# Kernel optimization log

Hardware: AMD Instinct MI355X
Metric: run time of the kernel (lower is better)

The kernel has to match this reference:

```python
import jax, jax.numpy as jnp
import numpy as np
from math import ceil

EPS = 1e-5
K_NN = 4
RATIO = 0.8


def _bn(x, g, b, rm, rv):
    # BatchNorm1d in inference mode with running stats
    return (x - rm) * (g / jnp.sqrt(rv + EPS)) + b


def _mlp1(x, W, bias, g, b, rm, rv):
    # S(Linear, ReLU, BN)
    return _bn(jax.nn.relu(x @ W + bias), g, b, rm, rv)


def _knn_edges(pos, B, n, k):
    p = pos.reshape(B, n, -1)
    d2 = jnp.sum((p[:, :, None, :] - p[:, None, :, :]) ** 2, axis=-1)  # [B,n,n]
    d2 = d2 + jnp.eye(n, dtype=d2.dtype) * 1e10  # loop=False
    _, nbr = jax.lax.top_k(-d2, k)  # [B,n,k] k nearest neighbors j of node i
    off = (jnp.arange(B, dtype=jnp.int32) * n)[:, None, None]
    src = (nbr.astype(jnp.int32) + off).reshape(-1)  # sources j (x_j)
    dst = (jnp.broadcast_to(jnp.arange(n, dtype=jnp.int32)[None, :, None], (B, n, k)) + off).reshape(-1)  # targets i (x_i)
    return src, dst


def _edge_conv(x, src, dst, emask, N, W, bias, g, b, rm, rv):
    xi = x[dst]
    xj = x[src]
    m = _mlp1(jnp.concatenate([xi, xj - xi], axis=1), W, bias, g, b, rm, rv)
    m = m * emask[:, None]
    s = jax.ops.segment_sum(m, dst, num_segments=N)
    cnt = jax.ops.segment_sum(emask, dst, num_segments=N)
    return s / jnp.maximum(cnt, 1.0)[:, None]  # aggr='mean' (0 for isolated nodes)


def _topk_pool(x, src, dst, emask, w, B, n, k_keep):
    score = (x @ w) / jnp.linalg.norm(w)  # [B*n]
    top_sc, perm = jax.lax.top_k(score.reshape(B, n), k_keep)  # [B,k_keep]
    off = (jnp.arange(B, dtype=jnp.int32) * n)[:, None]
    perm_flat = (perm.astype(jnp.int32) + off).reshape(-1)
    x_new = x[perm_flat] * jnp.tanh(top_sc).reshape(-1)[:, None]
    old2new = jnp.full((B * n,), -1, dtype=jnp.int32).at[perm_flat].set(
        jnp.arange(B * k_keep, dtype=jnp.int32))
    ns, nd = old2new[src], old2new[dst]
    new_mask = emask * (ns >= 0).astype(emask.dtype) * (nd >= 0).astype(emask.dtype)
    return x_new, jnp.maximum(ns, 0), jnp.maximum(nd, 0), new_mask


def _forward(x, pos, B, n,
             W1, b1, g1, be1, rm1, rv1, pw1,
             W2, b2, g2, be2, rm2, rv2, pw2,
             W3, b3, g3, be3, rm3, rv3,
             Wc1, bc1, gc1, bec1, rmc1, rvc1,
             Wc2, bc2, gc2, bec2, rmc2, rvc2):
    src, dst = _knn_edges(pos, B, n, K_NN)
    emask = jnp.ones(src.shape[0], dtype=x.dtype)
    h = _edge_conv(x, src, dst, emask, B * n, W1, b1, g1, be1, rm1, rv1)
    k1 = ceil(RATIO * n)
    h, src, dst, emask = _topk_pool(h, src, dst, emask, pw1, B, n, k1)
    h = _edge_conv(h, src, dst, emask, B * k1, W2, b2, g2, be2, rm2, rv2)
    k2 = ceil(RATIO * k1)
    h, src, dst, emask = _topk_pool(h, src, dst, emask, pw2, B, k1, k2)
    h = _edge_conv(h, src, dst, emask, B * k2, W3, b3, g3, be3, rm3, rv3)
    gmp = h.reshape(B, k2, -1).mean(axis=1)  # global_mean_pool
    z = _mlp1(gmp, Wc1, bc1, gc1, bec1, rmc1, rvc1)
    z = _mlp1(z, Wc2, bc2, gc2, bec2, rmc2, rvc2)
    return jax.nn.sigmoid(z)[:, 0]


def setup_inputs() -> dict:
    key = jax.random.key(0)
    B, n, C = 256, 128, 53
    keys = iter(jax.random.split(key, 64))

    def nrm(shape, s=1.0):
        return jax.random.normal(next(keys), shape, jnp.float32) * s

    def lin(i, o):
        return nrm((i, o), 1.0 / np.sqrt(i)), nrm((o,), 0.01)

    def bnp(c):
        return (1.0 + nrm((c,), 0.1), nrm((c,), 0.1), nrm((c,), 0.1),
                0.5 + jax.random.uniform(next(keys), (c,), jnp.float32))

    inp = {"x": nrm((B * n, C)), "pos": nrm((B * n, 3))}
    inp["W1"], inp["b1"] = lin(106, 128)
    inp["g1"], inp["be1"], inp["rm1"], inp["rv1"] = bnp(128)
    inp["pw1"] = nrm((128,))
    inp["W2"], inp["b2"] = lin(256, 256)
    inp["g2"], inp["be2"], inp["rm2"], inp["rv2"] = bnp(256)
    inp["pw2"] = nrm((256,))
    inp["W3"], inp["b3"] = lin(512, 512)
    inp["g3"], inp["be3"], inp["rm3"], inp["rv3"] = bnp(512)
    inp["Wc1"], inp["bc1"] = lin(512, 512)
    inp["gc1"], inp["bec1"], inp["rmc1"], inp["rvc1"] = bnp(512)
    inp["Wc2"], inp["bc2"] = lin(512, 1)
    inp["gc2"], inp["bec2"], inp["rmc2"], inp["rvc2"] = bnp(1)
    inp["n_graphs"] = B
    inp["nodes_per_graph"] = n
    return inp


def reference(x, pos,
              W1, b1, g1, be1, rm1, rv1, pw1,
              W2, b2, g2, be2, rm2, rv2, pw2,
              W3, b3, g3, be3, rm3, rv3,
              Wc1, bc1, gc1, bec1, rmc1, rvc1,
              Wc2, bc2, gc2, bec2, rmc2, rvc2,
              n_graphs, nodes_per_graph):
    return _forward(x, pos, n_graphs, nodes_per_graph,
                    W1, b1, g1, be1, rm1, rv1, pw1,
                    W2, b2, g2, be2, rm2, rv2, pw2,
                    W3, b3, g3, be3, rm3, rv3,
                    Wc1, bc1, gc1, bec1, rmc1, rvc1,
                    Wc2, bc2, gc2, bec2, rmc2, rvc2)
```

## Files before the change

### kernel.cpp

```cpp
#include <hip/hip_runtime.h>
#include <hip/hip_bf16.h>
#include <math.h>

#define B_G  256
#define NPG  128
#define KNN_ 4
#define CIN  53
#define N1   32768
#define KP1  103
#define N2   26368
#define KP2  83
#define N3   21248
#define O1   128
#define O2   256
#define O3   512
#define EPSB 1e-5f

typedef __attribute__((ext_vector_type(8))) short bf16x8;
typedef __attribute__((ext_vector_type(4))) float f32x4;

__device__ inline ushort f2bf(float f) {
    unsigned u = __builtin_bit_cast(unsigned, f);
    u += 0x7fff + ((u >> 16) & 1);
    return (ushort)(u >> 16);
}
__device__ inline float bf2f(ushort h) {
    unsigned u = ((unsigned)h) << 16;
    return __builtin_bit_cast(float, u);
}

__global__ void pack_w_k(const float* __restrict__ W, float* __restrict__ Wp,
                         int Kd, int O) {
    int i = blockIdx.x * blockDim.x + threadIdx.x;
    int tot = Kd * 2 * O;
    if (i >= tot) return;
    int k = i / (2 * O), c = i % (2 * O);
    Wp[i] = (c < O) ? W[k * O + c] : W[(Kd + k) * O + (c - O)];
}

__global__ void pack_w3t_k(const float* __restrict__ W3,
                           ushort* __restrict__ BhT, ushort* __restrict__ BlT) {
    int i = blockIdx.x * blockDim.x + threadIdx.x;
    if (i >= 1024 * 256) return;
    int n = i >> 8, k = i & 255;
    float w = (n < 512) ? W3[(size_t)k * 512 + n] : W3[(size_t)(256 + k) * 512 + (n - 512)];
    ushort h = f2bf(w);
    BhT[i] = h;
    BlT[i] = f2bf(w - bf2f(h));
}

__global__ void norm_w_k(const float* __restrict__ pw, float* __restrict__ pwn, int O) {
    __shared__ float red[256];
    float s = 0.f;
    for (int c = threadIdx.x; c < O; c += 256) s += pw[c] * pw[c];
    red[threadIdx.x] = s;
    __syncthreads();
    for (int st = 128; st > 0; st >>= 1) {
        if (threadIdx.x < st) red[threadIdx.x] += red[threadIdx.x + st];
        __syncthreads();
    }
    float inv = 1.0f / sqrtf(red[0]);
    for (int c = threadIdx.x; c < O; c += 256) pwn[c] = pw[c] * inv;
}

__global__ void knn_k(const float* __restrict__ pos, int* __restrict__ nbr) {
    int g = blockIdx.x;
    int i = threadIdx.x;
    __shared__ float px[NPG], py[NPG], pz[NPG];
    const float* p = pos + (size_t)g * NPG * 3;
    px[i] = p[i * 3 + 0]; py[i] = p[i * 3 + 1]; pz[i] = p[i * 3 + 2];
    __syncthreads();
    float b0 = 1e30f, b1 = 1e30f, b2 = 1e30f, b3 = 1e30f;
    int   i0 = 0, i1 = 0, i2 = 0, i3 = 0;
    float xi = px[i], yi = py[i], zi = pz[i];
    for (int j = 0; j < NPG; ++j) {
        float dx = xi - px[j], dy = yi - py[j], dz = zi - pz[j];
        float d2 = dx * dx + dy * dy + dz * dz;
        if (j != i && d2 < b3) {
            if (d2 < b0) {
                b3 = b2; i3 = i2; b2 = b1; i2 = i1; b1 = b0; i1 = i0; b0 = d2; i0 = j;
            } else if (d2 < b1) {
                b3 = b2; i3 = i2; b2 = b1; i2 = i1; b1 = d2; i1 = j;
            } else if (d2 < b2) {
                b3 = b2; i3 = i2; b2 = d2; i2 = j;
            } else {
                b3 = d2; i3 = j;
            }
        }
    }
    int base = (g * NPG + i) * KNN_;
    nbr[base + 0] = g * NPG + i0;
    nbr[base + 1] = g * NPG + i1;
    nbr[base + 2] = g * NPG + i2;
    nbr[base + 3] = g * NPG + i3;
}

template <int VEC>
__global__ __launch_bounds__(256) void gemm128_k(
        const float* __restrict__ A, const float* __restrict__ Bm,
        float* __restrict__ Cm, int M, int N, int Kd, int lda) {
    __shared__ float As[16][128];
    __shared__ float Bs[16][128];
    const int tid = threadIdx.x;
    const int row0 = blockIdx.y * 128, col0 = blockIdx.x * 128;
    const int tx = tid & 15;
    const int ty = (tid >> 4) & 15;
    const int s_arow = tid >> 1, s_ak = (tid & 1) * 8;
    const int s_bk = tid >> 4, s_bc = (tid & 15) * 8;
    float acc[8][8] = {};
    for (int k0 = 0; k0 < Kd; k0 += 16) {
        if (VEC) {
            const float4* ap = (const float4*)(A + (size_t)(row0 + s_arow) * lda + k0 + s_ak);
            float4 a0 = ap[0], a1 = ap[1];
            As[s_ak + 0][s_arow] = a0.x; As[s_ak + 1][s_arow] = a0.y;
            As[s_ak + 2][s_arow] = a0.z; As[s_ak + 3][s_arow] = a0.w;
            As[s_ak + 4][s_arow] = a1.x; As[s_ak + 5][s_arow] = a1.y;
            As[s_ak + 6][s_arow] = a1.z; As[s_ak + 7][s_arow] = a1.w;
            const float4* bp = (const float4*)(Bm + (size_t)(k0 + s_bk) * N + col0 + s_bc);
            float4 b0 = bp[0], b1 = bp[1];
            *(float4*)&Bs[s_bk][s_bc] = b0;
            *(float4*)&Bs[s_bk][s_bc + 4] = b1;
        } else {
            #pragma unroll
            for (int s = 0; s < 8; ++s) {
                int kk = s_ak + s;
                As[kk][s_arow] = (k0 + kk < Kd)
                    ? A[(size_t)(row0 + s_arow) * lda + k0 + kk] : 0.f;
            }
            #pragma unroll
            for (int s = 0; s < 8; ++s) {
                Bs[s_bk][s_bc + s] = (k0 + s_bk < Kd)
                    ? Bm[(size_t)(k0 + s_bk) * N + col0 + s_bc + s] : 0.f;
            }
        }
        __syncthreads();
        #pragma unroll
        for (int kk = 0; kk < 16; ++kk) {
            float a[8], b[8];
            *(float4*)&a[0] = *(const float4*)&As[kk][ty * 4];
            *(float4*)&a[4] = *(const float4*)&As[kk][64 + ty * 4];
            *(float4*)&b[0] = *(const float4*)&Bs[kk][tx * 4];
            *(float4*)&b[4] = *(const float4*)&Bs[kk][64 + tx * 4];
            #pragma unroll
            for (int i = 0; i < 8; ++i)
                #pragma unroll
                for (int j = 0; j < 8; ++j)
                    acc[i][j] += a[i] * b[j];
        }
        __syncthreads();
    }
    #pragma unroll
    for (int i = 0; i < 8; ++i) {
        int r = row0 + ((i < 4) ? (ty * 4 + i) : (64 + ty * 4 + (i - 4)));
        size_t base = (size_t)r * N + col0;
        *(float4*)&Cm[base + tx * 4]      = *(float4*)&acc[i][0];
        *(float4*)&Cm[base + 64 + tx * 4] = *(float4*)&acc[i][4];
    }
}

#define LDK 40
__global__ __launch_bounds__(256) void gemm3_mfma_k(
        const ushort* __restrict__ Ah, const ushort* __restrict__ Al,
        const ushort* __restrict__ BhT, const ushort* __restrict__ BlT,
        float* __restrict__ Cm) {
    __shared__ ushort sAh[128][LDK], sAl[128][LDK], sBh[128][LDK], sBl[128][LDK];
    const int tid = threadIdx.x;
    const int row0 = blockIdx.y * 128, col0 = blockIdx.x * 128;
    const int w = tid >> 6, lane = tid & 63;
    const int wr = (w >> 1) * 64, wc = (w & 1) * 64;
    const int fr = lane & 15, fk = (lane >> 4) * 8;
    const int s_r = tid >> 2, s_c = (tid & 3) * 8;
    f32x4 acc[4][4] = {};
    for (int k0 = 0; k0 < 256; k0 += 32) {
        {
            size_t ga0 = (size_t)(row0 + s_r) * 256 + k0 + s_c;
            size_t ga1 = (size_t)(row0 + 64 + s_r) * 256 + k0 + s_c;
            *(uint4*)&sAh[s_r][s_c]      = *(const uint4*)&Ah[ga0];
            *(uint4*)&sAh[64 + s_r][s_c] = *(const uint4*)&Ah[ga1];
            *(uint4*)&sAl[s_r][s_c]      = *(const uint4*)&Al[ga0];
            *(uint4*)&sAl[64 + s_r][s_c] = *(const uint4*)&Al[ga1];
            size_t gb0 = (size_t)(col0 + s_r) * 256 + k0 + s_c;
            size_t gb1 = (size_t)(col0 + 64 + s_r) * 256 + k0 + s_c;
            *(uint4*)&sBh[s_r][s_c]      = *(const uint4*)&BhT[gb0];
            *(uint4*)&sBh[64 + s_r][s_c] = *(const uint4*)&BhT[gb1];
            *(uint4*)&sBl[s_r][s_c]      = *(const uint4*)&BlT[gb0];
            *(uint4*)&sBl[64 + s_r][s_c] = *(const uint4*)&BlT[gb1];
        }
        __syncthreads();
        bf16x8 fa_h[4], fa_l[4], fb_h[4], fb_l[4];
        #pragma unroll
        for (int mi = 0; mi < 4; ++mi) {
            fa_h[mi] = *(const bf16x8*)&sAh[wr + mi * 16 + fr][fk];
            fa_l[mi] = *(const bf16x8*)&sAl[wr + mi * 16 + fr][fk];
        }
        #pragma unroll
        for (int ni = 0; ni < 4; ++ni) {
            fb_h[ni] = *(const bf16x8*)&sBh[wc + ni * 16 + fr][fk];
            fb_l[ni] = *(const bf16x8*)&sBl[wc + ni * 16 + fr][fk];
        }
        #pragma unroll
        for (int mi = 0; mi < 4; ++mi)
            #pragma unroll
            for (int ni = 0; ni < 4; ++ni) {
                acc[mi][ni] = __builtin_amdgcn_mfma_f32_16x16x32_bf16(
                    fa_h[mi], fb_h[ni], acc[mi][ni], 0, 0, 0);
                acc[mi][ni] = __builtin_amdgcn_mfma_f32_16x16x32_bf16(
                    fa_h[mi], fb_l[ni], acc[mi][ni], 0, 0, 0);
                acc[mi][ni] = __builtin_amdgcn_mfma_f32_16x16x32_bf16(
                    fa_l[mi], fb_h[ni], acc[mi][ni], 0, 0, 0);
            }
        __syncthreads();
    }
    const int crow = (lane >> 4) * 4, ccol = lane & 15;
    #pragma unroll
    for (int mi = 0; mi < 4; ++mi)
        #pragma unroll
        for (int ni = 0; ni < 4; ++ni) {
            size_t base = (size_t)(row0 + wr + mi * 16 + crow) * 1024
                          + col0 + wc + ni * 16 + ccol;
            #pragma unroll
            for (int r = 0; r < 4; ++r)
                Cm[base + (size_t)r * 1024] = acc[mi][ni][r];
        }
}

__global__ void conv_agg_k(const float* __restrict__ AC, const int* __restrict__ edges,
                           const float* __restrict__ bias, const float* __restrict__ g,
                           const float* __restrict__ be, const float* __restrict__ rm,
                           const float* __restrict__ rv, float* __restrict__ out, int O) {
    int node = blockIdx.x;
    int c = threadIdx.x;
    int e0 = node * KNN_;
    int j0 = edges[e0 + 0], j1 = edges[e0 + 1], j2 = edges[e0 + 2], j3 = edges[e0 + 3];
    size_t s2O = (size_t)2 * O;
    float Ai = AC[(size_t)node * s2O + c];
    float Ci = AC[(size_t)node * s2O + O + c];
    float base = Ai - Ci + bias[c];
    float acc = 0.f; int cnt = 0;
    if (j0 >= 0) { acc += fmaxf(base + AC[(size_t)j0 * s2O + O + c], 0.f); ++cnt; }
    if (j1 >= 0) { acc += fmaxf(base + AC[(size_t)j1 * s2O + O + c], 0.f); ++cnt; }
    if (j2 >= 0) { acc += fmaxf(base + AC[(size_t)j2 * s2O + O + c], 0.f); ++cnt; }
    if (j3 >= 0) { acc += fmaxf(base + AC[(size_t)j3 * s2O + O + c], 0.f); ++cnt; }
    float h;
    if (cnt > 0) {
        float m = acc / (float)cnt;
        float sc = g[c] / sqrtf(rv[c] + EPSB);
        h = (m - rm[c]) * sc + be[c];
    } else {
        h = 0.f;
    }
    out[(size_t)node * O + c] = h;
}

__global__ void score_k(const float* __restrict__ h, const float* __restrict__ pwn,
                        float* __restrict__ sc, int Nl, int O) {
    int wid = (blockIdx.x * blockDim.x + threadIdx.x) >> 6;
    int lane = threadIdx.x & 63;
    if (wid >= Nl) return;
    float s = 0.f;
    for (int c = lane; c < O; c += 64) s += h[(size_t)wid * O + c] * pwn[c];
    #pragma unroll
    for (int off = 32; off > 0; off >>= 1) s += __shfl_down(s, off);
    if (lane == 0) sc[wid] = s;
}

__global__ void topk_rank_k(const float* __restrict__ sc, int n_l, int k_keep,
                            float* __restrict__ gate, int* __restrict__ perm,
                            int* __restrict__ o2n) {
    int g = blockIdx.x;
    int t = threadIdx.x;
    __shared__ float s[NPG];
    if (t < n_l) s[t] = sc[(size_t)g * n_l + t];
    __syncthreads();
    if (t >= n_l) return;
    float v = s[t];
    int rank = 0;
    for (int j = 0; j < n_l; ++j) {
        float vj = s[j];
        rank += (vj > v || (vj == v && j < t)) ? 1 : 0;
    }
    int gi = g * n_l + t;
    if (rank < k_keep) {
        int d = g * k_keep + rank;
        perm[d] = gi;
        gate[d] = tanhf(v);
        o2n[gi] = d;
    } else {
        o2n[gi] = -1;
    }
}

__global__ void gather_k(const float* __restrict__ h, const int* __restrict__ perm,
                         const float* __restrict__ gate, float* __restrict__ xo,
                         int total, int oshift) {
    int i = blockIdx.x * blockDim.x + threadIdx.x;
    if (i >= total) return;
    int d = i >> oshift, c = i & ((1 << oshift) - 1);
    xo[i] = h[((size_t)perm[d] << oshift) + c] * gate[d];
}

__global__ void gather_bf_k(const float* __restrict__ h, const int* __restrict__ perm,
                            const float* __restrict__ gate,
                            ushort* __restrict__ Ah, ushort* __restrict__ Al, int total) {
    int i = blockIdx.x * blockDim.x + threadIdx.x;
    if (i >= total) return;
    int d = i >> 8, c = i & 255;
    float v = h[((size_t)perm[d] << 8) + c] * gate[d];
    ushort hh = f2bf(v);
    Ah[i] = hh;
    Al[i] = f2bf(v - bf2f(hh));
}

__global__ void build_e2_k(const int* __restrict__ nbr, const int* __restrict__ perm1,
                           const int* __restrict__ o2n1, int* __restrict__ e2, int total) {
    int i = blockIdx.x * blockDim.x + threadIdx.x;
    if (i >= total) return;
    int u = i >> 2, kk = i & 3;
    e2[i] = o2n1[nbr[perm1[u] * KNN_ + kk]];
}

__global__ void build_e3_k(const int* __restrict__ e2, const int* __restrict__ perm2,
                           const int* __restrict__ o2n2, int* __restrict__ e3, int total) {
    int i = blockIdx.x * blockDim.x + threadIdx.x;
    if (i >= total) return;
    int v = i >> 2, kk = i & 3;
    int s1 = e2[perm2[v] * KNN_ + kk];
    e3[i] = (s1 >= 0) ? o2n2[s1] : -1;
}

__global__ void gmp_k(const float* __restrict__ h3, float* __restrict__ gmp) {
    int g = blockIdx.x, c = threadIdx.x;
    float s = 0.f;
    for (int r = 0; r < KP2; ++r) s += h3[((size_t)(g * KP2 + r)) * O3 + c];
    gmp[(size_t)g * O3 + c] = s / (float)KP2;
}

__global__ void mlpc_k(const float* __restrict__ X, const float* __restrict__ W,
                       const float* __restrict__ bias, const float* __restrict__ g,
                       const float* __restrict__ be, const float* __restrict__ rm,
                       const float* __restrict__ rv, float* __restrict__ out) {
    int b = blockIdx.x, o = threadIdx.x;
    __shared__ float xr[512];
    xr[o] = X[(size_t)b * 512 + o];
    __syncthreads();
    float acc = bias[o];
    for (int k = 0; k < 512; ++k) acc += xr[k] * W[(size_t)k * 512 + o];
    acc = fmaxf(acc, 0.f);
    float s = g[o] / sqrtf(rv[o] + EPSB);
    out[(size_t)b * 512 + o] = (acc - rm[o]) * s + be[o];
}

__global__ void final_k(const float* __restrict__ z1, const float* __restrict__ Wc2,
                        const float* __restrict__ bc2, const float* __restrict__ gc2,
                        const float* __restrict__ bec2, const float* __restrict__ rmc2,
                        const float* __restrict__ rvc2, float* __restrict__ out) {
    int b = blockIdx.x * blockDim.x + threadIdx.x;
    if (b >= B_G) return;
    float acc = bc2[0];
    for (int k = 0; k < 512; ++k) acc += z1[(size_t)b * 512 + k] * Wc2[k];
    acc = fmaxf(acc, 0.f);
    float s = gc2[0] / sqrtf(rvc2[0] + EPSB);
    float z = (acc - rmc2[0]) * s + bec2[0];
    out[b] = 1.f / (1.f + expf(-z));
}

extern "C" void kernel_launch(void* const* d_in, const int* in_sizes, int n_in,
                              void* d_out, int out_size, void* d_ws, size_t ws_size,
                              hipStream_t stream) {
    const float* x    = (const float*)d_in[0];
    const float* pos  = (const float*)d_in[1];
    const float* W1   = (const float*)d_in[2];
    const float* b1   = (const float*)d_in[3];
    const float* g1   = (const float*)d_in[4];
    const float* be1  = (const float*)d_in[5];
    const float* rm1  = (const float*)d_in[6];
    const float* rv1  = (const float*)d_in[7];
    const float* pw1  = (const float*)d_in[8];
    const float* W2   = (const float*)d_in[9];
    const float* b2   = (const float*)d_in[10];
    const float* g2   = (const float*)d_in[11];
    const float* be2  = (const float*)d_in[12];
    const float* rm2  = (const float*)d_in[13];
    const float* rv2  = (const float*)d_in[14];
    const float* pw2  = (const float*)d_in[15];
    const float* W3   = (const float*)d_in[16];
    const float* b3   = (const float*)d_in[17];
    const float* g3   = (const float*)d_in[18];
    const float* be3  = (const float*)d_in[19];
    const float* rm3  = (const float*)d_in[20];
    const float* rv3  = (const float*)d_in[21];
    const float* Wc1  = (const float*)d_in[22];
    const float* bc1  = (const float*)d_in[23];
    const float* gc1  = (const float*)d_in[24];
    const float* bec1 = (const float*)d_in[25];
    const float* rmc1 = (const float*)d_in[26];
    const float* rvc1 = (const float*)d_in[27];
    const float* Wc2  = (const float*)d_in[28];
    const float* bc2  = (const float*)d_in[29];
    const float* gc2  = (const float*)d_in[30];
    const float* bec2 = (const float*)d_in[31];
    const float* rmc2 = (const float*)d_in[32];
    const float* rvc2 = (const float*)d_in[33];
    float* out = (float*)d_out;

    char* ws = (char*)d_ws;
    size_t off = 0;
    auto take = [&](size_t bytes) { size_t o = off; off = (off + bytes + 255) & ~(size_t)255; return o; };
    size_t o_nbr   = take((size_t)N1 * KNN_ * 4);
    size_t o_perm1 = take((size_t)N2 * 4);
    size_t o_o2n1  = take((size_t)N1 * 4);
    size_t o_perm2 = take((size_t)N3 * 4);
    size_t o_o2n2  = take((size_t)N2 * 4);
    size_t o_e2    = take((size_t)N2 * KNN_ * 4);
    size_t o_e3    = take((size_t)N3 * KNN_ * 4);
    size_t o_pwn1  = take((size_t)O1 * 4);
    size_t o_pwn2  = take((size_t)O2 * 4);
    size_t o_sc1   = take((size_t)N1 * 4);
    size_t o_sc2   = take((size_t)N2 * 4);
    size_t o_gate1 = take((size_t)N2 * 4);
    size_t o_gate2 = take((size_t)N3 * 4);
    size_t o_Wp1   = take((size_t)CIN * 2 * O1 * 4);
    size_t o_Wp2   = take((size_t)O1 * 2 * O2 * 4);
    size_t o_Bh3   = take((size_t)1024 * 256 * 2);
    size_t o_Bl3   = take((size_t)1024 * 256 * 2);
    size_t o_gmp   = take((size_t)B_G * O3 * 4);
    size_t o_z1    = take((size_t)B_G * O3 * 4);
    size_t o_S1    = take((size_t)N3 * 2 * O3 * 4);
    size_t o_S2    = take((size_t)N2 * 2 * O2 * 4);

    int*   nbr   = (int*)(ws + o_nbr);
    int*   perm1 = (int*)(ws + o_perm1);
    int*   o2n1  = (int*)(ws + o_o2n1);
    int*   perm2 = (int*)(ws + o_perm2);
    int*   o2n2  = (int*)(ws + o_o2n2);
    int*   e2    = (int*)(ws + o_e2);
    int*   e3    = (int*)(ws + o_e3);
    float* pwn1  = (float*)(ws + o_pwn1);
    float* pwn2  = (float*)(ws + o_pwn2);
    float* sc1   = (float*)(ws + o_sc1);
    float* sc2   = (float*)(ws + o_sc2);
    float* gate1 = (float*)(ws + o_gate1);
    float* gate2 = (float*)(ws + o_gate2);
    float* Wp1   = (float*)(ws + o_Wp1);
    float* Wp2   = (float*)(ws + o_Wp2);
    ushort* Bh3  = (ushort*)(ws + o_Bh3);
    ushort* Bl3  = (ushort*)(ws + o_Bl3);
    float* gmpb  = (float*)(ws + o_gmp);
    float* z1b   = (float*)(ws + o_z1);
    float* S1    = (float*)(ws + o_S1);
    float* S2    = (float*)(ws + o_S2);

    float* AC1 = S1;  float* h1  = S2;
    float* x1p = S1;  float* AC2 = S2;
    float* h2  = S1;
    ushort* x2h = (ushort*)S2;
    ushort* x2l = (ushort*)(S2 + (size_t)N3 * 256);
    float* AC3 = S1;  float* h3  = S2;

    pack_w_k<<<(CIN * 2 * O1 + 255) / 256, 256, 0, stream>>>(W1, Wp1, CIN, O1);
    pack_w_k<<<(O1 * 2 * O2 + 255) / 256, 256, 0, stream>>>(W2, Wp2, O1, O2);
    pack_w3t_k<<<(1024 * 256) / 256, 256, 0, stream>>>(W3, Bh3, Bl3);
    norm_w_k<<<1, 256, 0, stream>>>(pw1, pwn1, O1);
    norm_w_k<<<1, 256, 0, stream>>>(pw2, pwn2, O2);
    knn_k<<<B_G, NPG, 0, stream>>>(pos, nbr);

    gemm128_k<0><<<dim3(2 * O1 / 128, N1 / 128), 256, 0, stream>>>(
        x, Wp1, AC1, N1, 2 * O1, CIN, CIN);
    conv_agg_k<<<N1, O1, 0, stream>>>(AC1, nbr, b1, g1, be1, rm1, rv1, h1, O1);
    score_k<<<(N1 + 3) / 4, 256, 0, stream>>>(h1, pwn1, sc1, N1, O1);
    topk_rank_k<<<B_G, NPG, 0, stream>>>(sc1, NPG, KP1, gate1, perm1, o2n1);
    gather_k<<<(N2 * O1 + 255) / 256, 256, 0, stream>>>(h1, perm1, gate1, x1p, N2 * O1, 7);
    build_e2_k<<<(N2 * KNN_ + 255) / 256, 256, 0, stream>>>(nbr, perm1, o2n1, e2, N2 * KNN_);

    gemm128_k<1><<<dim3(2 * O2 / 128, N2 / 128), 256, 0, stream>>>(
        x1p, Wp2, AC2, N2, 2 * O2, O1, O1);
    conv_agg_k<<<N2, O2, 0, stream>>>(AC2, e2, b2, g2, be2, rm2, rv2, h2, O2);
    score_k<<<(N2 + 3) / 4, 256, 0, stream>>>(h2, pwn2, sc2, N2, O2);
    topk_rank_k<<<B_G, NPG, 0, stream>>>(sc2, KP1, KP2, gate2, perm2, o2n2);
    gather_bf_k<<<(N3 * O2 + 255) / 256, 256, 0, stream>>>(h2, perm2, gate2, x2h, x2l, N3 * O2);
    build_e3_k<<<(N3 * KNN_ + 255) / 256, 256, 0, stream>>>(e2, perm2, o2n2, e3, N3 * KNN_);

    gemm3_mfma_k<<<dim3(1024 / 128, N3 / 128), 256, 0, stream>>>(x2h, x2l, Bh3, Bl3, AC3);
    conv_agg_k<<<N3, O3, 0, stream>>>(AC3, e3, b3, g3, be3, rm3, rv3, h3, O3);

    gmp_k<<<B_G, O3, 0, stream>>>(h3, gmpb);
    mlpc_k<<<B_G, 512, 0, stream>>>(gmpb, Wc1, bc1, gc1, bec1, rmc1, rvc1, z1b);
    final_k<<<1, 256, 0, stream>>>(z1b, Wc2, bc2, gc2, bec2, rmc2, rvc2, out);
}
```

Before: 480.0 us.

## Fuse prep, topk+edge-build and readout kernels; move layer-2 GEMM to split-bf16 MFMA

Merges the weight packing and norm kernels into one prep kernel, fuses top-k ranking with edge remapping using shared-memory old-to-new maps, and fuses global mean pooling with both classifier layers into one readout kernel. The aim is to cut launch count and intermediate global buffers. The layer-2 GEMM now uses the templated split-bf16 (hi/lo) MFMA kernel instead of the fp32 SIMT GEMM, with a bf16 gather producing the split inputs. The three-product hi/lo scheme drops the lo*lo term, so small precision differences are possible.

```diff
diff --git a/kernel.cpp b/kernel.cpp
--- a/kernel.cpp
+++ b/kernel.cpp
@@ -29,38 +29,55 @@
     return __builtin_bit_cast(float, u);
 }
 
-__global__ void pack_w_k(const float* __restrict__ W, float* __restrict__ Wp,
-                         int Kd, int O) {
-    int i = blockIdx.x * blockDim.x + threadIdx.x;
-    int tot = Kd * 2 * O;
-    if (i >= tot) return;
-    int k = i / (2 * O), c = i % (2 * O);
-    Wp[i] = (c < O) ? W[k * O + c] : W[(Kd + k) * O + (c - O)];
-}
-
-__global__ void pack_w3t_k(const float* __restrict__ W3,
-                           ushort* __restrict__ BhT, ushort* __restrict__ BlT) {
-    int i = blockIdx.x * blockDim.x + threadIdx.x;
-    if (i >= 1024 * 256) return;
-    int n = i >> 8, k = i & 255;
-    float w = (n < 512) ? W3[(size_t)k * 512 + n] : W3[(size_t)(256 + k) * 512 + (n - 512)];
-    ushort h = f2bf(w);
-    BhT[i] = h;
-    BlT[i] = f2bf(w - bf2f(h));
-}
-
-__global__ void norm_w_k(const float* __restrict__ pw, float* __restrict__ pwn, int O) {
+__global__ void prep_k(const float* __restrict__ pw1, float* __restrict__ pwn1,
+                       const float* __restrict__ pw2, float* __restrict__ pwn2,
+                       const float* __restrict__ W1, float* __restrict__ Wp1,
+                       const float* __restrict__ W2,
+                       ushort* __restrict__ Bh2, ushort* __restrict__ Bl2,
+                       const float* __restrict__ W3,
+                       ushort* __restrict__ Bh3, ushort* __restrict__ Bl3) {
     __shared__ float red[256];
-    float s = 0.f;
-    for (int c = threadIdx.x; c < O; c += 256) s += pw[c] * pw[c];
-    red[threadIdx.x] = s;
-    __syncthreads();
-    for (int st = 128; st > 0; st >>= 1) {
-        if (threadIdx.x < st) red[threadIdx.x] += red[threadIdx.x + st];
+    if (blockIdx.x < 2) {
+        const float* pw = (blockIdx.x == 0) ? pw1 : pw2;
+        float* pwn      = (blockIdx.x == 0) ? pwn1 : pwn2;
+        int O           = (blockIdx.x == 0) ? O1 : O2;
+        float s = 0.f;
+        for (int c = threadIdx.x; c < O; c += 256) s += pw[c] * pw[c];
+        red[threadIdx.x] = s;
         __syncthreads();
-    }
-    float inv = 1.0f / sqrtf(red[0]);
-    for (int c = threadIdx.x; c < O; c += 256) pwn[c] = pw[c] * inv;
+        for (int st = 128; st > 0; st >>= 1) {
+            if (threadIdx.x < st) red[threadIdx.x] += red[threadIdx.x + st];
+            __syncthreads();
+        }
+        float inv = 1.0f / sqrtf(red[0]);
+        for (int c = threadIdx.x; c < O; c += 256) pwn[c] = pw[c] * inv;
+        return;
+    }
+    const int T2 = 512 * 128;
+    const int T3 = 1024 * 256;
+    const int T1 = CIN * 2 * O1;
+    int total = T2 + T3 + T1;
+    int stride = (gridDim.x - 2) * 256;
+    for (int idx = (blockIdx.x - 2) * 256 + threadIdx.x; idx < total; idx += stride) {
+        if (idx < T2) {
+            int n = idx >> 7, k = idx & 127;
+            float w = (n < 256) ? W2[(size_t)k * 256 + n]
+                                : W2[(size_t)(128 + k) * 256 + (n - 256)];
+            ushort h = f2bf(w);
+            Bh2[idx] = h; Bl2[idx] = f2bf(w - bf2f(h));
+        } else if (idx < T2 + T3) {
+            int j = idx - T2;
+            int n = j >> 8, k = j & 255;
+            float w = (n < 512) ? W3[(size_t)k * 512 + n]
+                                : W3[(size_t)(256 + k) * 512 + (n - 512)];
+            ushort h = f2bf(w);
+            Bh3[j] = h; Bl3[j] = f2bf(w - bf2f(h));
+        } else {
+            int j = idx - T2 - T3;
+            int k = j / (2 * O1), c = j % (2 * O1);
+            Wp1[j] = (c < O1) ? W1[k * O1 + c] : W1[(CIN + k) * O1 + (c - O1)];
+        }
+    }
 }
 
 __global__ void knn_k(const float* __restrict__ pos, int* __restrict__ nbr) {
@@ -159,7 +176,8 @@
 }
 
 #define LDK 40
-__global__ __launch_bounds__(256) void gemm3_mfma_k(
+template <int Kd, int Nc>
+__global__ __launch_bounds__(256) void gemm_mfma_k(
         const ushort* __restrict__ Ah, const ushort* __restrict__ Al,
         const ushort* __restrict__ BhT, const ushort* __restrict__ BlT,
         float* __restrict__ Cm) {
@@ -171,16 +189,16 @@
     const int fr = lane & 15, fk = (lane >> 4) * 8;
     const int s_r = tid >> 2, s_c = (tid & 3) * 8;
     f32x4 acc[4][4] = {};
-    for (int k0 = 0; k0 < 256; k0 += 32) {
+    for (int k0 = 0; k0 < Kd; k0 += 32) {
         {
-            size_t ga0 = (size_t)(row0 + s_r) * 256 + k0 + s_c;
-            size_t ga1 = (size_t)(row0 + 64 + s_r) * 256 + k0 + s_c;
+            size_t ga0 = (size_t)(row0 + s_r) * Kd + k0 + s_c;
+            size_t ga1 = (size_t)(row0 + 64 + s_r) * Kd + k0 + s_c;
             *(uint4*)&sAh[s_r][s_c]      = *(const uint4*)&Ah[ga0];
             *(uint4*)&sAh[64 + s_r][s_c] = *(const uint4*)&Ah[ga1];
             *(uint4*)&sAl[s_r][s_c]      = *(const uint4*)&Al[ga0];
             *(uint4*)&sAl[64 + s_r][s_c] = *(const uint4*)&Al[ga1];
-            size_t gb0 = (size_t)(col0 + s_r) * 256 + k0 + s_c;
-            size_t gb1 = (size_t)(col0 + 64 + s_r) * 256 + k0 + s_c;
+            size_t gb0 = (size_t)(col0 + s_r) * Kd + k0 + s_c;
+            size_t gb1 = (size_t)(col0 + 64 + s_r) * Kd + k0 + s_c;
             *(uint4*)&sBh[s_r][s_c]      = *(const uint4*)&BhT[gb0];
             *(uint4*)&sBh[64 + s_r][s_c] = *(const uint4*)&BhT[gb1];
             *(uint4*)&sBl[s_r][s_c]      = *(const uint4*)&BlT[gb0];
@@ -216,11 +234,11 @@
     for (int mi = 0; mi < 4; ++mi)
         #pragma unroll
         for (int ni = 0; ni < 4; ++ni) {
-            size_t base = (size_t)(row0 + wr + mi * 16 + crow) * 1024
+            size_t base = (size_t)(row0 + wr + mi * 16 + crow) * Nc
                           + col0 + wc + ni * 16 + ccol;
             #pragma unroll
             for (int r = 0; r < 4; ++r)
-                Cm[base + (size_t)r * 1024] = acc[mi][ni][r];
+                Cm[base + (size_t)r * Nc] = acc[mi][ni][r];
         }
 }
 
@@ -264,104 +282,86 @@
     if (lane == 0) sc[wid] = s;
 }
 
-__global__ void topk_rank_k(const float* __restrict__ sc, int n_l, int k_keep,
+__global__ void topk_edge_k(const float* __restrict__ sc, int n_l, int k_keep,
                             float* __restrict__ gate, int* __restrict__ perm,
-                            int* __restrict__ o2n) {
+                            const int* __restrict__ nbr_src, int* __restrict__ e_out) {
     int g = blockIdx.x;
     int t = threadIdx.x;
     __shared__ float s[NPG];
+    __shared__ int o2n_l[NPG], perm_l[NPG];
     if (t < n_l) s[t] = sc[(size_t)g * n_l + t];
     __syncthreads();
-    if (t >= n_l) return;
-    float v = s[t];
-    int rank = 0;
-    for (int j = 0; j < n_l; ++j) {
-        float vj = s[j];
-        rank += (vj > v || (vj == v && j < t)) ? 1 : 0;
-    }
-    int gi = g * n_l + t;
-    if (rank < k_keep) {
-        int d = g * k_keep + rank;
-        perm[d] = gi;
-        gate[d] = tanhf(v);
-        o2n[gi] = d;
-    } else {
-        o2n[gi] = -1;
-    }
-}
-
-__global__ void gather_k(const float* __restrict__ h, const int* __restrict__ perm,
-                         const float* __restrict__ gate, float* __restrict__ xo,
-                         int total, int oshift) {
-    int i = blockIdx.x * blockDim.x + threadIdx.x;
-    if (i >= total) return;
-    int d = i >> oshift, c = i & ((1 << oshift) - 1);
-    xo[i] = h[((size_t)perm[d] << oshift) + c] * gate[d];
-}
-
+    if (t < n_l) {
+        float v = s[t];
+        int rank = 0;
+        for (int j = 0; j < n_l; ++j) {
+            float vj = s[j];
+            rank += (vj > v || (vj == v && j < t)) ? 1 : 0;
+        }
+        int gi = g * n_l + t;
+        if (rank < k_keep) {
+            int d = g * k_keep + rank;
+            perm[d] = gi;
+            gate[d] = tanhf(v);
+            o2n_l[t] = d;
+            perm_l[rank] = gi;
+        } else {
+            o2n_l[t] = -1;
+        }
+    }
+    __syncthreads();
+    for (int u = t; u < k_keep; u += NPG) {
+        int old = perm_l[u];
+        #pragma unroll
+        for (int kk = 0; kk < KNN_; ++kk) {
+            int srcid = nbr_src[(size_t)old * KNN_ + kk];
+            int m = (srcid >= 0) ? o2n_l[srcid - g * n_l] : -1;
+            e_out[((size_t)(g * k_keep + u)) * KNN_ + kk] = m;
+        }
+    }
+}
+
+template <int OSH>
 __global__ void gather_bf_k(const float* __restrict__ h, const int* __restrict__ perm,
                             const float* __restrict__ gate,
                             ushort* __restrict__ Ah, ushort* __restrict__ Al, int total) {
     int i = blockIdx.x * blockDim.x + threadIdx.x;
     if (i >= total) return;
-    int d = i >> 8, c = i & 255;
-    float v = h[((size_t)perm[d] << 8) + c] * gate[d];
+    int d = i >> OSH, c = i & ((1 << OSH) - 1);
+    float v = h[((size_t)perm[d] << OSH) + c] * gate[d];
     ushort hh = f2bf(v);
     Ah[i] = hh;
     Al[i] = f2bf(v - bf2f(hh));
 }
 
-__global__ void build_e2_k(const int* __restrict__ nbr, const int* __restrict__ perm1,
-                           const int* __restrict__ o2n1, int* __restrict__ e2, int total) {
-    int i = blockIdx.x * blockDim.x + threadIdx.x;
-    if (i >= total) return;
-    int u = i >> 2, kk = i & 3;
-    e2[i] = o2n1[nbr[perm1[u] * KNN_ + kk]];
-}
-
-__global__ void build_e3_k(const int* __restrict__ e2, const int* __restrict__ perm2,
-                           const int* __restrict__ o2n2, int* __restrict__ e3, int total) {
-    int i = blockIdx.x * blockDim.x + threadIdx.x;
-    if (i >= total) return;
-    int v = i >> 2, kk = i & 3;
-    int s1 = e2[perm2[v] * KNN_ + kk];
-    e3[i] = (s1 >= 0) ? o2n2[s1] : -1;
-}
-
-__global__ void gmp_k(const float* __restrict__ h3, float* __restrict__ gmp) {
-    int g = blockIdx.x, c = threadIdx.x;
+__global__ void readout_k(const float* __restrict__ h3,
+                          const float* __restrict__ Wc1, const float* __restrict__ bc1,
+                          const float* __restrict__ gc1, const float* __restrict__ bec1,
+                          const float* __restrict__ rmc1, const float* __restrict__ rvc1,
+                          const float* __restrict__ Wc2, const float* __restrict__ bc2,
+                          const float* __restrict__ gc2, const float* __restrict__ bec2,
+                          const float* __restrict__ rmc2, const float* __restrict__ rvc2,
+                          float* __restrict__ out) {
+    int g = blockIdx.x, o = threadIdx.x;
+    __shared__ float xr[512], z1[512];
     float s = 0.f;
-    for (int r = 0; r < KP2; ++r) s += h3[((size_t)(g * KP2 + r)) * O3 + c];
-    gmp[(size_t)g * O3 + c] = s / (float)KP2;
-}
-
-__global__ void mlpc_k(const float* __restrict__ X, const float* __restrict__ W,
-                       const float* __restrict__ bias, const float* __restrict__ g,
-                       const float* __restrict__ be, const float* __restrict__ rm,
-                       const float* __restrict__ rv, float* __restrict__ out) {
-    int b = blockIdx.x, o = threadIdx.x;
-    __shared__ float xr[512];
-    xr[o] = X[(size_t)b * 512 + o];
+    for (int r = 0; r < KP2; ++r) s += h3[((size_t)(g * KP2 + r)) * O3 + o];
+    xr[o] = s / (float)KP2;
     __syncthreads();
-    float acc = bias[o];
-    for (int k = 0; k < 512; ++k) acc += xr[k] * W[(size_t)k * 512 + o];
+    float acc = bc1[o];
+    for (int k = 0; k < 512; ++k) acc += xr[k] * Wc1[(size_t)k * 512 + o];
     acc = fmaxf(acc, 0.f);
-    float s = g[o] / sqrtf(rv[o] + EPSB);
-    out[(size_t)b * 512 + o] = (acc - rm[o]) * s + be[o];
-}
-
-__global__ void final_k(const float* __restrict__ z1, const float* __restrict__ Wc2,
-                        const float* __restrict__ bc2, const float* __restrict__ gc2,
-                        const float* __restrict__ bec2, const float* __restrict__ rmc2,
-                        const float* __restrict__ rvc2, float* __restrict__ out) {
-    int b = blockIdx.x * blockDim.x + threadIdx.x;
-    if (b >= B_G) return;
-    float acc = bc2[0];
-    for (int k = 0; k < 512; ++k) acc += z1[(size_t)b * 512 + k] * Wc2[k];
-    acc = fmaxf(acc, 0.f);
-    float s = gc2[0] / sqrtf(rvc2[0] + EPSB);
-    float z = (acc - rmc2[0]) * s + bec2[0];
-    out[b] = 1.f / (1.f + expf(-z));
+    float sc1v = gc1[o] / sqrtf(rvc1[o] + EPSB);
+    z1[o] = (acc - rmc1[o]) * sc1v + bec1[o];
+    __syncthreads();
+    if (o == 0) {
+        float a = bc2[0];
+        for (int k = 0; k < 512; ++k) a += z1[k] * Wc2[k];
+        a = fmaxf(a, 0.f);
+        float sc2v = gc2[0] / sqrtf(rvc2[0] + EPSB);
+        float z = (a - rmc2[0]) * sc2v + bec2[0];
+        out[g] = 1.f / (1.f + expf(-z));
+    }
 }
 
 extern "C" void kernel_launch(void* const* d_in, const int* in_sizes, int n_in,
@@ -408,9 +408,7 @@
     auto take = [&](size_t bytes) { size_t o = off; off = (off + bytes + 255) & ~(size_t)255; return o; };
     size_t o_nbr   = take((size_t)N1 * KNN_ * 4);
     size_t o_perm1 = take((size_t)N2 * 4);
-    size_t o_o2n1  = take((size_t)N1 * 4);
     size_t o_perm2 = take((size_t)N3 * 4);
-    size_t o_o2n2  = take((size_t)N2 * 4);
     size_t o_e2    = take((size_t)N2 * KNN_ * 4);
     size_t o_e3    = take((size_t)N3 * KNN_ * 4);
     size_t o_pwn1  = take((size_t)O1 * 4);
@@ -420,19 +418,16 @@
     size_t o_gate1 = take((size_t)N2 * 4);
     size_t o_gate2 = take((size_t)N3 * 4);
     size_t o_Wp1   = take((size_t)CIN * 2 * O1 * 4);
-    size_t o_Wp2   = take((size_t)O1 * 2 * O2 * 4);
+    size_t o_Bh2   = take((size_t)512 * 128 * 2);
+    size_t o_Bl2   = take((size_t)512 * 128 * 2);
     size_t o_Bh3   = take((size_t)1024 * 256 * 2);
     size_t o_Bl3   = take((size_t)1024 * 256 * 2);
-    size_t o_gmp   = take((size_t)B_G * O3 * 4);
-    size_t o_z1    = take((size_t)B_G * O3 * 4);
     size_t o_S1    = take((size_t)N3 * 2 * O3 * 4);
     size_t o_S2    = take((size_t)N2 * 2 * O2 * 4);
 
     int*   nbr   = (int*)(ws + o_nbr);
     int*   perm1 = (int*)(ws + o_perm1);
-    int*   o2n1  = (int*)(ws + o_o2n1);
     int*   perm2 = (int*)(ws + o_perm2);
-    int*   o2n2  = (int*)(ws + o_o2n2);
     int*   e2    = (int*)(ws + o_e2);
     int*   e3    = (int*)(ws + o_e3);
     float* pwn1  = (float*)(ws + o_pwn1);
@@ -442,48 +437,47 @@
     float* gate1 = (float*)(ws + o_gate1);
     float* gate2 = (float*)(ws + o_gate2);
     float* Wp1   = (float*)(ws + o_Wp1);
-    float* Wp2   = (float*)(ws + o_Wp2);
+    ushort* Bh2  = (ushort*)(ws + o_Bh2);
+    ushort* Bl2  = (ushort*)(ws + o_Bl2);
     ushort* Bh3  = (ushort*)(ws + o_Bh3);
     ushort* Bl3  = (ushort*)(ws + o_Bl3);
-    float* gmpb  = (float*)(ws + o_gmp);
-    float* z1b   = (float*)(ws + o_z1);
     float* S1    = (float*)(ws + o_S1);
     float* S2    = (float*)(ws + o_S2);
 
     float* AC1 = S1;  float* h1  = S2;
-    float* x1p = S1;  float* AC2 = S2;
+    ushort* x1h = (ushort*)S1;
+    ushort* x1l = x1h + (size_t)N2 * O1;
+    float* AC2 = S2;
     float* h2  = S1;
     ushort* x2h = (ushort*)S2;
-    ushort* x2l = (ushort*)(S2 + (size_t)N3 * 256);
-    float* AC3 = S1;  float* h3  = S2;
-
-    pack_w_k<<<(CIN * 2 * O1 + 255) / 256, 256, 0, stream>>>(W1, Wp1, CIN, O1);
-    pack_w_k<<<(O1 * 2 * O2 + 255) / 256, 256, 0, stream>>>(W2, Wp2, O1, O2);
-    pack_w3t_k<<<(1024 * 256) / 256, 256, 0, stream>>>(W3, Bh3, Bl3);
-    norm_w_k<<<1, 256, 0, stream>>>(pw1, pwn1, O1);
-    norm_w_k<<<1, 256, 0, stream>>>(pw2, pwn2, O2);
+    ushort* x2l = x2h + (size_t)N3 * O2;
+    float* AC3 = S1;
+    float* h3  = S2;
+
+    prep_k<<<258, 256, 0, stream>>>(pw1, pwn1, pw2, pwn2, W1, Wp1,
+                                    W2, Bh2, Bl2, W3, Bh3, Bl3);
     knn_k<<<B_G, NPG, 0, stream>>>(pos, nbr);
 
     gemm128_k<0><<<dim3(2 * O1 / 128, N1 / 128), 256, 0, stream>>>(
         x, Wp1, AC1, N1, 2 * O1, CIN, CIN);
     conv_agg_k<<<N1, O1, 0, stream>>>(AC1, nbr, b1, g1, be1, rm1, rv1, h1, O1);
     score_k<<<(N1 + 3) / 4, 256, 0, stream>>>(h1, pwn1, sc1, N1, O1);
-    topk_rank_k<<<B_G, NPG, 0, stream>>>(sc1, NPG, KP1, gate1, perm1, o2n1);
-    gather_k<<<(N2 * O1 + 255) / 256, 256, 0, stream>>>(h1, perm1, gate1, x1p, N2 * O1, 7);
-    build_e2_k<<<(N2 * KNN_ + 255) / 256, 256, 0, stream>>>(nbr, perm1, o2n1, e2, N2 * KNN_);
-
-    gemm128_k<1><<<dim3(2 * O2 / 128, N2 / 128), 256, 0, stream>>>(
-        x1p, Wp2, AC2, N2, 2 * O2, O1, O1);
+    topk_edge_k<<<B_G, NPG, 0, stream>>>(sc1, NPG, KP1, gate1, perm1, nbr, e2);
+    gather_bf_k<7><<<(N2 * O1 + 255) / 256, 256, 0, stream>>>(
+        h1, perm1, gate1, x1h, x1l, N2 * O1);
+
+    gemm_mfma_k<O1, 2 * O2><<<dim3(2 * O2 / 128, N2 / 128), 256, 0, stream>>>(
+        x1h, x1l, Bh2, Bl2, AC2);
     conv_agg_k<<<N2, O2, 0, stream>>>(AC2, e2, b2, g2, be2, rm2, rv2, h2, O2);
     score_k<<<(N2 + 3) / 4, 256, 0, stream>>>(h2, pwn2, sc2, N2, O2);
-    topk_rank_k<<<B_G, NPG, 0, stream>>>(sc2, KP1, KP2, gate2, perm2, o2n2);
-    gather_bf_k<<<(N3 * O2 + 255) / 256, 256, 0, stream>>>(h2, perm2, gate2, x2h, x2l, N3 * O2);
-    build_e3_k<<<(N3 * KNN_ + 255) / 256, 256, 0, stream>>>(e2, perm2, o2n2, e3, N3 * KNN_);
-
-    gemm3_mfma_k<<<dim3(1024 / 128, N3 / 128), 256, 0, stream>>>(x2h, x2l, Bh3, Bl3, AC3);
+    topk_edge_k<<<B_G, NPG, 0, stream>>>(sc2, KP1, KP2, gate2, perm2, e2, e3);
+    gather_bf_k<8><<<(N3 * O2 + 255) / 256, 256, 0, stream>>>(
+        h2, perm2, gate2, x2h, x2l, N3 * O2);
+
+    gemm_mfma_k<O2, 2 * O3><<<dim3(2 * O3 / 128, N3 / 128), 256, 0, stream>>>(
+        x2h, x2l, Bh3, Bl3, AC3);
     conv_agg_k<<<N3, O3, 0, stream>>>(AC3, e3, b3, g3, be3, rm3, rv3, h3, O3);
 
-    gmp_k<<<B_G, O3, 0, stream>>>(h3, gmpb);
-    mlpc_k<<<B_G, 512, 0, stream>>>(gmpb, Wc1, bc1, gc1, bec1, rmc1, rvc1, z1b);
-    final_k<<<1, 256, 0, stream>>>(z1b, Wc2, bc2, gc2, bec2, rmc2, rvc2, out);
-}
+    readout_k<<<B_G, 512, 0, stream>>>(h3, Wc1, bc1, gc1, bec1, rmc1, rvc1,
+                                       Wc2, bc2, gc2, bec2, rmc2, rvc2, out);
+}
```

Result: faster. 429.5 us (-10.5%).
